# Optimization experiments

Hardware: AMD Instinct MI355X
Metric: run time of the kernel (lower is better)

Reference implementation:

```python
import jax, jax.numpy as jnp
import numpy as np

B, N, D = 8, 2048, 512  # batch, input_dim (tokens), weight_dim


def setup_inputs() -> dict:
    key = jax.random.key(0)
    ks = jax.random.split(key, 7)
    return {
        "query": jax.random.normal(ks[0], (B, N, D), dtype=jnp.float32),
        "key": jax.random.normal(ks[1], (B, N, D), dtype=jnp.float32),
        "value": jax.random.normal(ks[2], (B, N, D), dtype=jnp.float32),
        "W_query": jax.random.normal(ks[3], (D, D), dtype=jnp.float32),
        "W_key": jax.random.normal(ks[4], (D, D), dtype=jnp.float32),
        "W_value": jax.random.normal(ks[5], (D, D), dtype=jnp.float32),
        "self_importance": jnp.zeros((N,), dtype=jnp.float32),
    }


def reference(query, key, value, W_query, W_key, W_value, self_importance):
    d = W_query.shape[0]
    q = jnp.einsum("bnd,de->bne", query, W_query)
    k = jnp.einsum("bnd,de->bne", key, W_key)
    v = jnp.einsum("bnd,de->bne", value, W_value)
    scores = jnp.einsum("bqe,bke->bqk", q, k) / jnp.sqrt(jnp.float32(d))
    # diagonal self-importance bias: eye(N) * clamp(exp(s), max=3)
    importance = jnp.minimum(jnp.exp(self_importance), 3.0)  # [N]
    n = scores.shape[1]
    idx = jnp.arange(n)
    scores = scores.at[:, idx, idx].add(importance)
    attn = jax.nn.softmax(scores, axis=-1)  # [B, N, N]
    entropy_loss = -jnp.mean(jnp.sum(attn * jnp.log(attn + 1e-10), axis=-1))
    out = jnp.einsum("bqk,bke->bqe", attn, v)
    return (out, attn, entropy_loss)
```

## Files before the change

### kernel.cpp

```cpp
#include <hip/hip_runtime.h>
#include <math.h>

#define BB 8
#define NN 2048
#define DD 512

typedef _Float16 halfT;
typedef _Float16 half8 __attribute__((ext_vector_type(8)));
typedef _Float16 half4 __attribute__((ext_vector_type(4)));
typedef float f32x4 __attribute__((ext_vector_type(4)));

#define GLOAD16(gp, sp) __builtin_amdgcn_global_load_lds( \
    (const __attribute__((address_space(1))) void*)(gp), \
    (__attribute__((address_space(3))) void*)(sp), 16, 0, 0)

__global__ __launch_bounds__(256) void wsplit_kernel(
    const float* __restrict__ Wq, const float* __restrict__ Wk, const float* __restrict__ Wv,
    _Float16* __restrict__ qhT, _Float16* __restrict__ qlT,
    _Float16* __restrict__ khT, _Float16* __restrict__ klT,
    _Float16* __restrict__ vhT)
{
    __shared__ float t[64][65];
    const int z = blockIdx.z;
    const float* W = (z == 0) ? Wq : ((z == 1) ? Wk : Wv);
    _Float16* Ph = (z == 0) ? qhT : ((z == 1) ? khT : vhT);
    _Float16* Pl = (z == 0) ? qlT : ((z == 1) ? klT : nullptr);
    const int bx = blockIdx.x * 64, by = blockIdx.y * 64;
    const int tid = threadIdx.x;
    #pragma unroll
    for (int i = 0; i < 16; ++i) {
        const int idx = i * 256 + tid;
        const int r = idx >> 6, c = idx & 63;
        t[r][c] = W[(long)(by + r) * 512 + bx + c];
    }
    __syncthreads();
    #pragma unroll
    for (int i = 0; i < 16; ++i) {
        const int idx = i * 256 + tid;
        const int r = idx >> 6, c = idx & 63;
        const float v = t[c][r];
        const _Float16 h = (_Float16)v;
        const long o = (long)(bx + r) * 512 + by + c;
        Ph[o] = h;
        if (z < 2) Pl[o] = (_Float16)(v - (float)h);
    }
}

__global__ __launch_bounds__(256) void proj_kernel(
    const float* __restrict__ X0, const float* __restrict__ X1, const float* __restrict__ X2,
    const halfT* __restrict__ B0h, const halfT* __restrict__ B0l,
    const halfT* __restrict__ B1h, const halfT* __restrict__ B1l,
    const halfT* __restrict__ B2h,
    halfT* __restrict__ O0h, halfT* __restrict__ O0l,
    halfT* __restrict__ O1h, halfT* __restrict__ O1l,
    halfT* __restrict__ O2)
{
    __shared__ __align__(16) char smem[32768];

    const int tid  = threadIdx.x;
    const int lane = tid & 63;
    const int w    = tid >> 6;
    const int wr   = w >> 1, wc = w & 1;

    int h = blockIdx.x;
    h = (h & 7) * 192 + (h >> 3);
    int z, nx, my;
    if (h < 1024) { z = h >> 9; const int r = h & 511; nx = r & 3; my = r >> 2; }
    else          { const int r = h - 1024; z = 2;     nx = r & 3; my = r >> 2; }
    const int bm = my * 128, bn = nx * 128;
    const bool full = (z < 2);

    const float* X = (z == 0) ? X0 : ((z == 1) ? X1 : X2);
    const halfT* Bgh = (z == 0) ? B0h : ((z == 1) ? B1h : B2h);
    const halfT* Bgl = (z == 0) ? B0l : B1l;
    halfT* Oh = (z == 0) ? O0h : O1h;
    halfT* Ol = (z == 0) ? O0l : O1l;

    const int b_row   = w * 16 + (lane >> 2);
    const int b_chunk = (lane & 3) ^ ((lane >> 3) & 3);
    const long gB0 = (long)(bn + b_row) * DD + b_chunk * 8;
    const long gB1 = (long)(bn + b_row + 64) * DD + b_chunk * 8;
    const int ldstB = w * 1024;

    const int a_row = tid >> 1;
    const int g0    = (tid & 1) << 1;
    const int aswz  = (a_row >> 1) & 3;
    const int p0 = g0 ^ aswz, p1 = (g0 + 1) ^ aswz;
    const long gA = (long)(bm + a_row) * DD + g0 * 8;
    const int aOff0 = a_row * 64 + p0 * 16;
    const int aOff1 = a_row * 64 + p1 * 16;

    float ar[16];
    auto loadA = [&](int t) {
        const long kk = (long)t * 32;
        *(float4*)&ar[0]  = *(const float4*)(X + gA + kk);
        *(float4*)&ar[4]  = *(const float4*)(X + gA + kk + 4);
        *(float4*)&ar[8]  = *(const float4*)(X + gA + kk + 8);
        *(float4*)&ar[12] = *(const float4*)(X + gA + kk + 12);
    };
    auto stageB = [&](int t) {
        const long kk = (long)t * 32;
        GLOAD16(Bgh + gB0 + kk, smem + 16384 + ldstB);
        GLOAD16(Bgh + gB1 + kk, smem + 16384 + 4096 + ldstB);
        if (full) {
            GLOAD16(Bgl + gB0 + kk, smem + 24576 + ldstB);
            GLOAD16(Bgl + gB1 + kk, smem + 24576 + 4096 + ldstB);
        }
    };
    auto writeA = [&]() {
        half8 h0, h1;
        #pragma unroll
        for (int i = 0; i < 8; ++i) h0[i] = (_Float16)ar[i];
        #pragma unroll
        for (int i = 0; i < 8; ++i) h1[i] = (_Float16)ar[8 + i];
        *(half8*)(smem + aOff0) = h0;
        *(half8*)(smem + aOff1) = h1;
        if (full) {
            half8 l0, l1;
            #pragma unroll
            for (int i = 0; i < 8; ++i) l0[i] = (_Float16)(ar[i] - (float)h0[i]);
            #pragma unroll
            for (int i = 0; i < 8; ++i) l1[i] = (_Float16)(ar[8 + i] - (float)h1[i]);
            *(half8*)(smem + 8192 + aOff0) = l0;
            *(half8*)(smem + 8192 + aOff1) = l1;
        }
    };

    const int lr  = lane & 15;
    const int q16 = lane >> 4;
    const int frag = lr * 64 + ((q16 ^ ((lr >> 1) & 3)) << 4);
    const int abase = wr * 4096 + frag;
    const int bbase = wc * 4096 + frag;

    f32x4 acc[4][4];
    #pragma unroll
    for (int i = 0; i < 4; ++i)
        #pragma unroll
        for (int j = 0; j < 4; ++j) acc[i][j] = (f32x4)0.0f;

    loadA(0);

    for (int t = 0; t < 16; ++t) {
        writeA();
        stageB(t);
        if (t < 15) loadA(t + 1);
        __syncthreads();

        half8 ah[4], bh[4];
        #pragma unroll
        for (int m = 0; m < 4; ++m)
            ah[m] = *(const half8*)(smem + abase + m * 1024);
        #pragma unroll
        for (int j = 0; j < 4; ++j)
            bh[j] = *(const half8*)(smem + 16384 + bbase + j * 1024);
        __builtin_amdgcn_s_setprio(1);
        #pragma unroll
        for (int m = 0; m < 4; ++m)
            #pragma unroll
            for (int j = 0; j < 4; ++j)
                acc[m][j] = __builtin_amdgcn_mfma_f32_16x16x32_f16(ah[m], bh[j], acc[m][j], 0, 0, 0);
        __builtin_amdgcn_s_setprio(0);

        if (full) {
            half8 bl[4];
            #pragma unroll
            for (int j = 0; j < 4; ++j)
                bl[j] = *(const half8*)(smem + 24576 + bbase + j * 1024);
            __builtin_amdgcn_s_setprio(1);
            #pragma unroll
            for (int m = 0; m < 4; ++m)
                #pragma unroll
                for (int j = 0; j < 4; ++j)
                    acc[m][j] = __builtin_amdgcn_mfma_f32_16x16x32_f16(ah[m], bl[j], acc[m][j], 0, 0, 0);
            __builtin_amdgcn_s_setprio(0);

            __builtin_amdgcn_s_setprio(1);
            #pragma unroll
            for (int m = 0; m < 4; ++m) {
                const half8 al = *(const half8*)(smem + 8192 + abase + m * 1024);
                #pragma unroll
                for (int j = 0; j < 4; ++j)
                    acc[m][j] = __builtin_amdgcn_mfma_f32_16x16x32_f16(al, bh[j], acc[m][j], 0, 0, 0);
            }
            __builtin_amdgcn_s_setprio(0);
        }
        __syncthreads();
    }

    if (full) {
        #pragma unroll
        for (int m = 0; m < 4; ++m) {
            const int rb = bm + wr * 64 + m * 16 + (q16 << 2);
            #pragma unroll
            for (int j = 0; j < 4; ++j) {
                const int gc = bn + wc * 64 + j * 16 + lr;
                #pragma unroll
                for (int r = 0; r < 4; ++r) {
                    const float vv = acc[m][j][r];
                    const _Float16 hh = (_Float16)vv;
                    const long o = (long)(rb + r) * DD + gc;
                    Oh[o] = hh;
                    Ol[o] = (_Float16)(vv - (float)hh);
                }
            }
        }
    } else {
        #pragma unroll
        for (int m = 0; m < 4; ++m) {
            const int rb = bm + wr * 64 + m * 16 + (q16 << 2);
            #pragma unroll
            for (int j = 0; j < 4; ++j) {
                const int gc = bn + wc * 64 + j * 16 + lr;
                half4 hv;
                #pragma unroll
                for (int r = 0; r < 4; ++r) hv[r] = (_Float16)acc[m][j][r];
                const int b = rb >> 11, rIn = rb & 2047;
                *(half4*)&O2[((long)b * 512 + gc) * 2048 + rIn] = hv;
            }
        }
    }
}

__global__ __launch_bounds__(512, 2) void scores256_kernel(
    const halfT* __restrict__ qh, const halfT* __restrict__ ql,
    const halfT* __restrict__ kh, const halfT* __restrict__ kl,
    float* __restrict__ C, const float* __restrict__ si, float scale)
{
    extern __shared__ __align__(16) char smem[];

    const int tid  = threadIdx.x;
    const int lane = tid & 63;
    const int w    = tid >> 6;
    const int wr   = w >> 2, wc = w & 3;

    int flat = (blockIdx.z << 6) | (blockIdx.y << 3) | blockIdx.x;
    flat = ((flat & 7) << 6) | (flat >> 3);
    const int bx = flat & 7, by = (flat >> 3) & 7, bz = flat >> 6;
    const int bm = by * 256, bn = bx * 256;

    const long zoff = (long)bz * NN * DD;
    const halfT* A_h = qh + zoff;
    const halfT* A_l = ql + zoff;
    const halfT* B_h = kh + zoff;
    const halfT* B_l = kl + zoff;

    const int s_row   = w * 16 + (lane >> 2);
    const int s_chunk = (lane & 3) ^ ((lane >> 3) & 3);
    const long gA = (long)(bm + s_row) * DD + s_chunk * 8;
    const long gB = (long)(bn + s_row) * DD + s_chunk * 8;
    const int ldst = w * 1024;
    const long rstep = (long)128 * DD;

    auto stage = [&](char* buf, int t) {
        const long kk = (long)t * 32;
        GLOAD16(A_h + gA + kk,         buf + ldst);
        GLOAD16(A_h + gA + rstep + kk, buf + 8192 + ldst);
        GLOAD16(A_l + gA + kk,         buf + 16384 + ldst);
        GLOAD16(A_l + gA + rstep + kk, buf + 16384 + 8192 + ldst);
        GLOAD16(B_h + gB + kk,         buf + 32768 + ldst);
        GLOAD16(B_h + gB + rstep + kk, buf + 32768 + 8192 + ldst);
        GLOAD16(B_l + gB + kk,         buf + 49152 + ldst);
        GLOAD16(B_l + gB + rstep + kk, buf + 49152 + 8192 + ldst);
    };

    const int lr   = lane & 15;
    const int q16  = lane >> 4;
    const int fswz = (lr >> 1) & 3;
    const int frag = lr * 64 + ((q16 ^ fswz) << 4);
    const int abase = wr * 8192 + frag;
    const int bbase = wc * 4096 + frag;

    f32x4 acc[8][4];
    #pragma unroll
    for (int m = 0; m < 8; ++m)
        #pragma unroll
        for (int n = 0; n < 4; ++n) acc[m][n] = (f32x4)0.0f;

    stage(smem, 0);
    asm volatile("s_waitcnt vmcnt(0)" ::: "memory");
    __builtin_amdgcn_s_barrier();

    for (int t = 0; t < 16; ++t) {
        char* cur = smem + (size_t)(t & 1) * 65536;
        char* nxt = smem + (size_t)((t + 1) & 1) * 65536;

        if (t < 15) stage(nxt, t + 1);

        half8 ah[8], bh[4], bl[4];
        #pragma unroll
        for (int n = 0; n < 4; ++n)
            bh[n] = *(const half8*)(cur + 32768 + bbase + n * 1024);
        #pragma unroll
        for (int m = 0; m < 8; ++m)
            ah[m] = *(const half8*)(cur + abase + m * 1024);
        __builtin_amdgcn_s_setprio(1);
        #pragma unroll
        for (int m = 0; m < 8; ++m)
            #pragma unroll
            for (int n = 0; n < 4; ++n)
                acc[m][n] = __builtin_amdgcn_mfma_f32_16x16x32_f16(ah[m], bh[n], acc[m][n], 0, 0, 0);
        __builtin_amdgcn_s_setprio(0);

        #pragma unroll
        for (int n = 0; n < 4; ++n)
            bl[n] = *(const half8*)(cur + 49152 + bbase + n * 1024);
        __builtin_amdgcn_s_setprio(1);
        #pragma unroll
        for (int m = 0; m < 8; ++m)
            #pragma unroll
            for (int n = 0; n < 4; ++n)
                acc[m][n] = __builtin_amdgcn_mfma_f32_16x16x32_f16(ah[m], bl[n], acc[m][n], 0, 0, 0);
        __builtin_amdgcn_s_setprio(0);

        __builtin_amdgcn_s_setprio(1);
        #pragma unroll
        for (int m = 0; m < 8; ++m) {
            const half8 al = *(const half8*)(cur + 16384 + abase + m * 1024);
            #pragma unroll
            for (int n = 0; n < 4; ++n)
                acc[m][n] = __builtin_amdgcn_mfma_f32_16x16x32_f16(al, bh[n], acc[m][n], 0, 0, 0);
        }
        __builtin_amdgcn_s_setprio(0);

        if (t < 15) {
            asm volatile("s_waitcnt vmcnt(0)" ::: "memory");
            __builtin_amdgcn_s_barrier();
        }
    }

    float* Cz = C + (long)bz * NN * NN;
    #pragma unroll
    for (int m = 0; m < 8; ++m) {
        const int rb = bm + wr * 128 + m * 16 + ((lane >> 4) << 2);
        #pragma unroll
        for (int n = 0; n < 4; ++n) {
            const int gc = bn + wc * 64 + n * 16 + (lane & 15);
            #pragma unroll
            for (int r = 0; r < 4; ++r) {
                const int gr = rb + r;
                float vv = acc[m][n][r] * scale;
                if (gr == gc) vv += fminf(expf(si[gr]), 3.0f);
                Cz[(long)gr * NN + gc] = vv;
            }
        }
    }
}

__global__ __launch_bounds__(512, 2) void av_kernel(
    const halfT* __restrict__ P, const halfT* __restrict__ V,
    float* __restrict__ O)
{
    extern __shared__ __align__(16) char smem[];

    const int tid  = threadIdx.x;
    const int lane = tid & 63;
    const int w    = tid >> 6;
    const int wr   = w >> 1, wc = w & 1;

    int flat = blockIdx.x;
    flat = ((flat & 7) << 5) | (flat >> 3);
    const int nx = flat & 3, my = (flat >> 2) & 7, bz = flat >> 5;
    const int bm = my * 256, bn = nx * 128;

    const halfT* A = P + (long)bz * NN * NN;
    const halfT* B = V + (long)bz * DD * NN;

    const int s_row   = w * 16 + (lane >> 2);
    const int s_chunk = (lane & 3) ^ ((lane >> 3) & 3);
    const long gA = (long)(bm + s_row) * NN + s_chunk * 8;
    const long gB = (long)(bn + s_row) * NN + s_chunk * 8;
    const int ldst = w * 1024;
    const long rstep = (long)128 * NN;

    auto stage = [&](char* buf, int t) {
        const long kk = (long)t * 32;
        GLOAD16(A + gA + kk,         buf + ldst);
        GLOAD16(A + gA + rstep + kk, buf + 8192 + ldst);
        GLOAD16(B + gB + kk,         buf + 16384 + ldst);
    };

    const int lr  = lane & 15;
    const int q16 = lane >> 4;
    const int frag = lr * 64 + ((q16 ^ ((lr >> 1) & 3)) << 4);
    const int abase = wr * 4096 + frag;
    const int bbase = wc * 4096 + frag;

    f32x4 acc[4][4];
    #pragma unroll
    for (int m = 0; m < 4; ++m)
        #pragma unroll
        for (int j = 0; j < 4; ++j) acc[m][j] = (f32x4)0.0f;

    stage(smem, 0);
    stage(smem + 24576, 1);
    asm volatile("s_waitcnt vmcnt(3)" ::: "memory");
    __builtin_amdgcn_s_barrier();
    __builtin_amdgcn_sched_barrier(0);

    int cb = 0;
    for (int t = 0; t < 64; ++t) {
        char* cur = smem + (size_t)cb * 24576;
        const int nb = (cb + 2 >= 3) ? cb - 1 : cb + 2;
        if (t < 62) stage(smem + (size_t)nb * 24576, t + 2);

        half8 ah[4], bh[4];
        #pragma unroll
        for (int m = 0; m < 4; ++m)
            ah[m] = *(const half8*)(cur + abase + m * 1024);
        #pragma unroll
        for (int j = 0; j < 4; ++j)
            bh[j] = *(const half8*)(cur + 16384 + bbase + j * 1024);
        __builtin_amdgcn_s_setprio(1);
        #pragma unroll
        for (int m = 0; m < 4; ++m)
            #pragma unroll
            for (int j = 0; j < 4; ++j)
                acc[m][j] = __builtin_amdgcn_mfma_f32_16x16x32_f16(ah[m], bh[j], acc[m][j], 0, 0, 0);
        __builtin_amdgcn_s_setprio(0);

        if (t < 63) {
            if (t < 62) { asm volatile("s_waitcnt vmcnt(3)" ::: "memory"); }
            else        { asm volatile("s_waitcnt vmcnt(0)" ::: "memory"); }
            __builtin_amdgcn_s_barrier();
            __builtin_amdgcn_sched_barrier(0);
        }
        cb = (cb + 1 == 3) ? 0 : cb + 1;
    }

    float* Oz = O + (long)bz * NN * DD;
    #pragma unroll
    for (int m = 0; m < 4; ++m) {
        const int rb = bm + wr * 64 + m * 16 + (q16 << 2);
        #pragma unroll
        for (int j = 0; j < 4; ++j) {
            const int gc = bn + wc * 64 + j * 16 + lr;
            #pragma unroll
            for (int r = 0; r < 4; ++r)
                Oz[(long)(rb + r) * DD + gc] = acc[m][j][r];
        }
    }
}

__global__ __launch_bounds__(256) void softmax_entropy_kernel(
    float* __restrict__ attn, _Float16* __restrict__ ah, float* __restrict__ partials)
{
    __shared__ float red[4];
    const long row = blockIdx.x;
    float* p = attn + row * (long)NN;
    _Float16* ph = ah + row * (long)NN;
    const int tid = threadIdx.x;
    const int base = tid * 8;

    float4 va = *(const float4*)(p + base);
    float4 vb = *(const float4*)(p + base + 4);
    float v[8] = {va.x, va.y, va.z, va.w, vb.x, vb.y, vb.z, vb.w};

    float m = v[0];
    #pragma unroll
    for (int i = 1; i < 8; ++i) m = fmaxf(m, v[i]);
    #pragma unroll
    for (int o = 32; o; o >>= 1) m = fmaxf(m, __shfl_xor(m, o, 64));
    if ((tid & 63) == 0) red[tid >> 6] = m;
    __syncthreads();
    m = fmaxf(fmaxf(red[0], red[1]), fmaxf(red[2], red[3]));

    float t[8];
    float s = 0.f;
    #pragma unroll
    for (int i = 0; i < 8; ++i) { t[i] = v[i] - m; v[i] = expf(t[i]); s += v[i]; }
    #pragma unroll
    for (int o = 32; o; o >>= 1) s += __shfl_xor(s, o, 64);
    __syncthreads();
    if ((tid & 63) == 0) red[tid >> 6] = s;
    __syncthreads();
    s = red[0] + red[1] + red[2] + red[3];

    const float inv = 1.0f / s;
    const float lns = logf(s);
    float e = 0.f;
    float pv[8];
    #pragma unroll
    for (int i = 0; i < 8; ++i) {
        pv[i] = v[i] * inv;
        e = fmaf(pv[i], t[i] - lns, e);
    }
    *(float4*)(p + base)     = make_float4(pv[0], pv[1], pv[2], pv[3]);
    *(float4*)(p + base + 4) = make_float4(pv[4], pv[5], pv[6], pv[7]);
    half8 h;
    #pragma unroll
    for (int i = 0; i < 8; ++i) h[i] = (_Float16)pv[i];
    *(half8*)(ph + base) = h;

    #pragma unroll
    for (int o = 32; o; o >>= 1) e += __shfl_xor(e, o, 64);
    __syncthreads();
    if ((tid & 63) == 0) red[tid >> 6] = e;
    __syncthreads();
    if (tid == 0) partials[row] = red[0] + red[1] + red[2] + red[3];
}

__global__ __launch_bounds__(256) void ent_reduce_kernel(
    const float* __restrict__ partials, float* __restrict__ ent)
{
    __shared__ float red[4];
    float s = 0.f;
    for (int i = threadIdx.x; i < BB * NN; i += 256) s += partials[i];
    #pragma unroll
    for (int o = 32; o; o >>= 1) s += __shfl_xor(s, o, 64);
    if ((threadIdx.x & 63) == 0) red[threadIdx.x >> 6] = s;
    __syncthreads();
    if (threadIdx.x == 0)
        *ent = -(red[0] + red[1] + red[2] + red[3]) / (float)(BB * NN);
}

extern "C" void kernel_launch(void* const* d_in, const int* in_sizes, int n_in,
                              void* d_out, int out_size, void* d_ws, size_t ws_size,
                              hipStream_t stream) {
    const float* query = (const float*)d_in[0];
    const float* key   = (const float*)d_in[1];
    const float* value = (const float*)d_in[2];
    const float* Wq    = (const float*)d_in[3];
    const float* Wk    = (const float*)d_in[4];
    const float* Wv    = (const float*)d_in[5];
    const float* si    = (const float*)d_in[6];

    float* out  = (float*)d_out;
    float* attn = out + (size_t)BB * NN * DD;
    float* ent  = attn + (size_t)BB * NN * NN;

    const size_t NK = (size_t)BB * NN * DD;
    _Float16* ws16 = (_Float16*)d_ws;
    _Float16* qh = ws16;
    _Float16* ql = qh + NK;
    _Float16* kh = ql + NK;
    _Float16* kl = kh + NK;
    _Float16* vT = kl + NK;
    _Float16* WqhT = vT + NK;
    _Float16* WqlT = WqhT + DD * DD;
    _Float16* WkhT = WqlT + DD * DD;
    _Float16* WklT = WkhT + DD * DD;
    _Float16* WvhT = WklT + DD * DD;
    float* partials = (float*)(WvhT + DD * DD);
    _Float16* attn_h = ws16;

    const dim3 blk(256);
    const float inv_sqrt_d = 0.044194173824159216f;

    wsplit_kernel<<<dim3(8, 8, 3), blk, 0, stream>>>(Wq, Wk, Wv,
        WqhT, WqlT, WkhT, WklT, WvhT);

    proj_kernel<<<dim3(1536), blk, 0, stream>>>(
        query, key, value, WqhT, WqlT, WkhT, WklT, WvhT,
        qh, ql, kh, kl, vT);

    scores256_kernel<<<dim3(8, 8, 8), dim3(512), 131072, stream>>>(
        qh, ql, kh, kl, attn, si, inv_sqrt_d);

    softmax_entropy_kernel<<<dim3(BB * NN), blk, 0, stream>>>(attn, attn_h, partials);
    ent_reduce_kernel<<<dim3(1), blk, 0, stream>>>(partials, ent);

    av_kernel<<<dim3(256), dim3(512), 73728, stream>>>(attn_h, vT, out);
}
```

Baseline: 302.2 us.

## Double-buffer LDS in projection GEMM to overlap loads with MFMA

```diff
diff --git a/kernel.cpp b/kernel.cpp
--- a/kernel.cpp
+++ b/kernel.cpp
@@ -46,7 +46,7 @@
     }
 }
 
-__global__ __launch_bounds__(256) void proj_kernel(
+__global__ __launch_bounds__(256, 2) void proj_kernel(
     const float* __restrict__ X0, const float* __restrict__ X1, const float* __restrict__ X2,
     const halfT* __restrict__ B0h, const halfT* __restrict__ B0l,
     const halfT* __restrict__ B1h, const halfT* __restrict__ B1l,
@@ -55,7 +55,7 @@
     halfT* __restrict__ O1h, halfT* __restrict__ O1l,
     halfT* __restrict__ O2)
 {
-    __shared__ __align__(16) char smem[32768];
+    __shared__ __align__(16) char smem[65536];
 
     const int tid  = threadIdx.x;
     const int lane = tid & 63;
@@ -98,31 +98,31 @@
         *(float4*)&ar[8]  = *(const float4*)(X + gA + kk + 8);
         *(float4*)&ar[12] = *(const float4*)(X + gA + kk + 12);
     };
-    auto stageB = [&](int t) {
+    auto stageB = [&](char* buf, int t) {
         const long kk = (long)t * 32;
-        GLOAD16(Bgh + gB0 + kk, smem + 16384 + ldstB);
-        GLOAD16(Bgh + gB1 + kk, smem + 16384 + 4096 + ldstB);
+        GLOAD16(Bgh + gB0 + kk, buf + 16384 + ldstB);
+        GLOAD16(Bgh + gB1 + kk, buf + 16384 + 4096 + ldstB);
         if (full) {
-            GLOAD16(Bgl + gB0 + kk, smem + 24576 + ldstB);
-            GLOAD16(Bgl + gB1 + kk, smem + 24576 + 4096 + ldstB);
+            GLOAD16(Bgl + gB0 + kk, buf + 24576 + ldstB);
+            GLOAD16(Bgl + gB1 + kk, buf + 24576 + 4096 + ldstB);
         }
     };
-    auto writeA = [&]() {
+    auto writeA = [&](char* buf) {
         half8 h0, h1;
         #pragma unroll
         for (int i = 0; i < 8; ++i) h0[i] = (_Float16)ar[i];
         #pragma unroll
         for (int i = 0; i < 8; ++i) h1[i] = (_Float16)ar[8 + i];
-        *(half8*)(smem + aOff0) = h0;
-        *(half8*)(smem + aOff1) = h1;
+        *(half8*)(buf + aOff0) = h0;
+        *(half8*)(buf + aOff1) = h1;
         if (full) {
             half8 l0, l1;
             #pragma unroll
             for (int i = 0; i < 8; ++i) l0[i] = (_Float16)(ar[i] - (float)h0[i]);
             #pragma unroll
             for (int i = 0; i < 8; ++i) l1[i] = (_Float16)(ar[8 + i] - (float)h1[i]);
-            *(half8*)(smem + 8192 + aOff0) = l0;
-            *(half8*)(smem + 8192 + aOff1) = l1;
+            *(half8*)(buf + 8192 + aOff0) = l0;
+            *(half8*)(buf + 8192 + aOff1) = l1;
         }
     };
 
@@ -139,20 +139,26 @@
         for (int j = 0; j < 4; ++j) acc[i][j] = (f32x4)0.0f;
 
     loadA(0);
+    stageB(smem, 0);
+    writeA(smem);
+    asm volatile("s_waitcnt vmcnt(0) lgkmcnt(0)" ::: "memory");
+    __builtin_amdgcn_s_barrier();
+    __builtin_amdgcn_sched_barrier(0);
 
     for (int t = 0; t < 16; ++t) {
-        writeA();
-        stageB(t);
-        if (t < 15) loadA(t + 1);
-        __syncthreads();
+        char* cur = smem + (size_t)(t & 1) * 32768;
+        char* nxt = smem + (size_t)((t + 1) & 1) * 32768;
+        const bool pf = (t < 15);
+
+        if (pf) { loadA(t + 1); stageB(nxt, t + 1); }
 
         half8 ah[4], bh[4];
         #pragma unroll
         for (int m = 0; m < 4; ++m)
-            ah[m] = *(const half8*)(smem + abase + m * 1024);
+            ah[m] = *(const half8*)(cur + abase + m * 1024);
         #pragma unroll
         for (int j = 0; j < 4; ++j)
-            bh[j] = *(const half8*)(smem + 16384 + bbase + j * 1024);
+            bh[j] = *(const half8*)(cur + 16384 + bbase + j * 1024);
         __builtin_amdgcn_s_setprio(1);
         #pragma unroll
         for (int m = 0; m < 4; ++m)
@@ -165,7 +171,7 @@
             half8 bl[4];
             #pragma unroll
             for (int j = 0; j < 4; ++j)
-                bl[j] = *(const half8*)(smem + 24576 + bbase + j * 1024);
+                bl[j] = *(const half8*)(cur + 24576 + bbase + j * 1024);
             __builtin_amdgcn_s_setprio(1);
             #pragma unroll
             for (int m = 0; m < 4; ++m)
@@ -177,14 +183,18 @@
             __builtin_amdgcn_s_setprio(1);
             #pragma unroll
             for (int m = 0; m < 4; ++m) {
-                const half8 al = *(const half8*)(smem + 8192 + abase + m * 1024);
+                const half8 al = *(const half8*)(cur + 8192 + abase + m * 1024);
                 #pragma unroll
                 for (int j = 0; j < 4; ++j)
                     acc[m][j] = __builtin_amdgcn_mfma_f32_16x16x32_f16(al, bh[j], acc[m][j], 0, 0, 0);
             }
             __builtin_amdgcn_s_setprio(0);
         }
-        __syncthreads();
+
+        if (pf) writeA(nxt);
+        asm volatile("s_waitcnt vmcnt(0) lgkmcnt(0)" ::: "memory");
+        __builtin_amdgcn_s_barrier();
+        __builtin_amdgcn_sched_barrier(0);
     }
 
     if (full) {
```

After: 301.1 us. About the same (-0.4%).
